# Optimization experiments

Measured on AMD Instinct MI355X. Metric: run time of the kernel, lower is better.

## Reference

```python
import jax, jax.numpy as jnp
import numpy as np

EMBED = 256; HEADS = 8; LEVELS = 4; POINTS = 4; DIM = EMBED // HEADS


def _bilinear_gather(vflat, H, W, px, py):
    """grid_sample(mode='bilinear', padding='zeros', align_corners=False).
    vflat: (bs, heads, H*W, d); px, py: (bs, heads, nq, P) pixel coords.
    Returns (bs, heads, nq, P, d).
    """
    x0 = jnp.floor(px); y0 = jnp.floor(py)
    x1 = x0 + 1.0;      y1 = y0 + 1.0
    wx1 = px - x0; wx0 = 1.0 - wx1
    wy1 = py - y0; wy0 = 1.0 - wy1

    def corner(ix, iy, w):
        valid = (ix >= 0) & (ix <= W - 1) & (iy >= 0) & (iy <= H - 1)
        idx = (jnp.clip(iy, 0, H - 1) * W + jnp.clip(ix, 0, W - 1)).astype(jnp.int32)
        b, h, nq, P = idx.shape
        g = jnp.take_along_axis(vflat, idx.reshape(b, h, nq * P)[..., None], axis=2)
        g = g.reshape(b, h, nq, P, -1)
        return g * (w * valid)[..., None]

    return (corner(x0, y0, wx0 * wy0) + corner(x1, y0, wx1 * wy0)
            + corner(x0, y1, wx0 * wy1) + corner(x1, y1, wx1 * wy1))


def _ms_deform_attn(value4, shapes, loc, attn):
    """value4 (bs,nv,heads,D); loc (bs,nq,heads,L,P,2) in [0,1];
    attn (bs,nq,heads,L,P). Returns (bs,nq,heads*D)."""
    bs, nq = loc.shape[0], loc.shape[1]
    grids = 2.0 * loc - 1.0
    attn_t = jnp.transpose(attn, (0, 2, 1, 3, 4))  # (bs,heads,nq,L,P)
    out = jnp.zeros((bs, HEADS, nq, DIM), value4.dtype)
    start = 0
    for lvl in range(LEVELS):
        H, W = int(shapes[lvl, 0]), int(shapes[lvl, 1])
        v = value4[:, start:start + H * W]                 # (bs,HW,heads,D)
        vflat = jnp.transpose(v, (0, 2, 1, 3))             # (bs,heads,HW,D)
        g = jnp.transpose(grids[:, :, :, lvl], (0, 2, 1, 3, 4))  # (bs,heads,nq,P,2)
        px = (g[..., 0] + 1.0) * (W * 0.5) - 0.5
        py = (g[..., 1] + 1.0) * (H * 0.5) - 0.5
        sampled = _bilinear_gather(vflat, H, W, px, py)    # (bs,heads,nq,P,D)
        out = out + jnp.einsum('bhqpd,bhqp->bhqd', sampled, attn_t[:, :, :, lvl])
        start += H * W
    return jnp.transpose(out, (0, 2, 1, 3)).reshape(bs, nq, HEADS * DIM)


def _forward(query, value, query_pos, reference_points, last_reference_offsets,
             shapes, Wv, bv, Wo, bo, Wa, ba, Wout, bout):
    identity = query
    q = query + query_pos
    bs, nq, _ = q.shape
    nv = value.shape[1]
    v = (value @ Wv + bv).reshape(bs, nv, HEADS, DIM)
    off = (q @ Wo + bo).reshape(bs, nq, HEADS, LEVELS, POINTS, 2)
    attn = jax.nn.softmax((q @ Wa + ba).reshape(bs, nq, HEADS, LEVELS * POINTS), axis=-1)
    attn = attn.reshape(bs, nq, HEADS, LEVELS, POINTS)
    wh = jnp.asarray(np.asarray(shapes)[:, ::-1].copy(), jnp.float32)  # (L,2) as (w,h)
    loc = (reference_points[:, :, None, :, None, :]
           + off / wh[None, None, None, :, None, :]
           + last_reference_offsets[:, :, :, None, None, :])  # flow-guided per-head shift
    out = _ms_deform_attn(v, shapes, loc, attn)
    return out @ Wout + bout + identity  # dropout is identity at eval


def setup_inputs() -> dict:
    key = jax.random.key(0)
    ks = jax.random.split(key, 10)
    bs, nq = 8, 1200
    shapes = np.array([[92, 160], [46, 80], [23, 40], [12, 20]], np.int64)
    nv = int((shapes[:, 0] * shapes[:, 1]).sum())
    f = jnp.float32
    return {
        "query": jax.random.normal(ks[0], (bs, nq, EMBED), f),
        "value": jax.random.normal(ks[1], (bs, nv, EMBED), f),
        "query_pos": jax.random.normal(ks[2], (bs, nq, EMBED), f),
        "reference_points": jax.random.uniform(ks[3], (bs, nq, LEVELS, 2), f),
        "last_reference_offsets": jax.random.normal(ks[4], (bs, nq, HEADS, 2), f) * 0.02,
        "spatial_shapes": shapes,
        "Wv": jax.random.normal(ks[5], (EMBED, EMBED), f) * 0.02,
        "bv": jnp.zeros((EMBED,), f),
        "Wo": jax.random.normal(ks[6], (EMBED, HEADS * LEVELS * POINTS * 2), f) * 0.02,
        "bo": jax.random.normal(ks[7], (HEADS * LEVELS * POINTS * 2,), f) * 0.02,
        "Wa": jax.random.normal(ks[8], (EMBED, HEADS * LEVELS * POINTS), f) * 0.02,
        "ba": jnp.zeros((HEADS * LEVELS * POINTS,), f),
        "Wout": jax.random.normal(ks[9], (EMBED, EMBED), f) * 0.02,
        "bout": jnp.zeros((EMBED,), f),
    }


def reference(query, value, query_pos, reference_points, last_reference_offsets,
              spatial_shapes, Wv, bv, Wo, bo, Wa, ba, Wout, bout):
    return _forward(query, value, query_pos, reference_points, last_reference_offsets,
                    spatial_shapes, Wv, bv, Wo, bo, Wa, ba, Wout, bout)
```

## Files before the change

kernel.cpp:

```cpp
#include <hip/hip_runtime.h>
#include <math.h>

#define BS 8
#define NQ 1200
#define NV 19560
#define EMB 256

typedef __bf16 bf16;
typedef bf16 bf16x8 __attribute__((ext_vector_type(8)));
typedef float f32x4 __attribute__((ext_vector_type(4)));
typedef float f32x16 __attribute__((ext_vector_type(16)));

static __device__ __forceinline__ bf16x8 cvt8(float4 a, float4 b) {
    bf16x8 r;
    r[0] = (bf16)a.x; r[1] = (bf16)a.y; r[2] = (bf16)a.z; r[3] = (bf16)a.w;
    r[4] = (bf16)b.x; r[5] = (bf16)b.y; r[6] = (bf16)b.z; r[7] = (bf16)b.w;
    return r;
}

static __device__ __forceinline__ void gl16(const void* g, void* l) {
    __builtin_amdgcn_global_load_lds(
        (const __attribute__((address_space(1))) void*)g,
        (__attribute__((address_space(3))) void*)l, 16, 0, 0);
}

__global__ __launch_bounds__(256) void prep_k(
    const float* __restrict__ Wv, const float* __restrict__ Wo,
    const float* __restrict__ Wa, const float* __restrict__ Wout,
    const float* __restrict__ query, const float* __restrict__ qpos,
    bf16* __restrict__ Wv_p, bf16* __restrict__ Wo_p,
    bf16* __restrict__ Wa_p, bf16* __restrict__ Wout_p, bf16* __restrict__ qsum)
{
    int bid = blockIdx.x, tid = threadIdx.x;
    if (bid < 896) {
        const float* src; bf16* dst; int N, t0;
        if (bid < 256)      { src = Wv;   dst = Wv_p;   N = 256; t0 = bid * 256; }
        else if (bid < 512) { src = Wo;   dst = Wo_p;   N = 256; t0 = (bid - 256) * 256; }
        else if (bid < 640) { src = Wa;   dst = Wa_p;   N = 128; t0 = (bid - 512) * 256; }
        else                { src = Wout; dst = Wout_p; N = 256; t0 = (bid - 640) * 256; }
        int t = t0 + tid;
        int n = t >> 8, k = t & 255;
        dst[t] = (bf16)src[k * N + n];
    } else {
        int t = (bid - 896) * 256 + tid;
        qsum[t] = (bf16)(query[t] + qpos[t]);
    }
}

__global__ __launch_bounds__(256, 1) void vgemm_k(
    const float* __restrict__ A, const bf16* __restrict__ Bp,
    const float* __restrict__ bias, bf16* __restrict__ outB, int Mtiles)
{
    __shared__ __align__(16) bf16 sB[256 * 256];
    __shared__ __align__(16) float sA[2][64 * 64];
    const int tid = threadIdx.x;
    const int lane = tid & 63;
    const int w = tid >> 6;
    const int l32 = lane & 31;
    const int hi = lane >> 5;
    const int wr = w >> 1, wc = w & 1;
    const int tstride = gridDim.x;

#pragma unroll
    for (int i = 0; i < 32; ++i) {
        int s = i * 256 + tid;
        int r = s >> 5, p = s & 31, c = p ^ (r & 7);
        gl16(Bp + (size_t)r * 256 + c * 8, sB + ((size_t)i * 256 + w * 64) * 8);
    }

    const int rl = lane >> 4;
    const int sl = lane & 15;
    auto stageA = [&](int t, int kc, int buf) {
        const float* base = A + (size_t)t * 64 * 256 + kc * 64;
#pragma unroll
        for (int i = 0; i < 4; ++i) {
            int r = w * 16 + i * 4 + rl;
            int c = sl ^ (r & 7);
            gl16(base + (size_t)r * 256 + c * 4, &sA[buf][(w * 16 + i * 4) * 64]);
        }
    };

    int t = blockIdx.x;
    stageA(t, 0, 0);

    float bb[4];
#pragma unroll
    for (int ct = 0; ct < 4; ++ct) bb[ct] = bias[wc * 128 + ct * 32 + l32];

    __syncthreads();

    int cur = 0;
    const int ar = wr * 32 + l32;
    while (true) {
        f32x16 acc[4];
#pragma unroll
        for (int ct = 0; ct < 4; ++ct)
#pragma unroll
            for (int rg = 0; rg < 16; ++rg) acc[ct][rg] = 0.f;

        const bool last = (t + tstride >= Mtiles);
#pragma unroll
        for (int kc = 0; kc < 4; ++kc) {
            if (kc < 3)     stageA(t, kc + 1, cur ^ 1);
            else if (!last) stageA(t + tstride, 0, cur ^ 1);
#pragma unroll
            for (int ks2 = 0; ks2 < 4; ++ks2) {
                int c0 = ks2 * 4 + hi * 2;
                float4 a0 = *(const float4*)&sA[cur][ar * 64 + ((c0    ) ^ (ar & 7)) * 4];
                float4 a1 = *(const float4*)&sA[cur][ar * 64 + ((c0 + 1) ^ (ar & 7)) * 4];
                bf16x8 af = cvt8(a0, a1);
                int p = ((kc * 4 + ks2) * 2 + hi) ^ (l32 & 7);
#pragma unroll
                for (int ct = 0; ct < 4; ++ct) {
                    int br = wc * 128 + ct * 32 + l32;
                    bf16x8 bfr = *(const bf16x8*)(sB + (size_t)br * 256 + p * 8);
                    acc[ct] = __builtin_amdgcn_mfma_f32_32x32x16_bf16(af, bfr, acc[ct], 0, 0, 0);
                }
            }
            __syncthreads();
            cur ^= 1;
        }

#pragma unroll
        for (int ct = 0; ct < 4; ++ct) {
            int col = wc * 128 + ct * 32 + l32;
#pragma unroll
            for (int rg = 0; rg < 16; ++rg) {
                int row = t * 64 + wr * 32 + (rg & 3) + 8 * (rg >> 2) + 4 * hi;
                outB[(size_t)row * 256 + col] = (bf16)(acc[ct][rg] + bb[ct]);
            }
        }
        if (last) break;
        t += tstride;
    }
}

template <int NS, int NB, bool HAS_RES, bool OUT_BF16>
__global__ __launch_bounds__(256, 2) void gemm3_k(
    const bf16* __restrict__ Ah, const bf16* __restrict__ Bp,
    const float* __restrict__ bias, const float* __restrict__ res,
    float* __restrict__ outF, bf16* __restrict__ outB, int Mtiles)
{
    constexpr int CT = NB / 16;
    __shared__ __align__(16) bf16 sB[NB * 256];
    const int tid = threadIdx.x;
    const int lane = tid & 63;
    const int w = tid >> 6;
    const int l16 = lane & 15;
    const int qd = lane >> 4;
    const int col0 = (blockIdx.x & 1) * NB;
    const int tstride = gridDim.x >> 1;
    const bf16* Bsrc = Bp + (size_t)col0 * 256;

    uint4 curH[8], nxtH[8];
    auto loadA = [&](int t, uint4* dH) {
        size_t rb = ((size_t)t * 64 + w * 16 + l16) * 256;
#pragma unroll
        for (int kc = 0; kc < 8; ++kc)
            dH[kc] = *(const uint4*)(Ah + rb + kc * 32 + qd * 8);
    };

    int tile = blockIdx.x >> 1;
    if (tile < Mtiles) loadA(tile, curH);

#pragma unroll
    for (int i = 0; i < NB * 32 / 256; ++i) {
        int s = i * 256 + tid;
        int r = s >> 5, p = s & 31, c = p ^ (r & 7);
        gl16(Bsrc + (size_t)r * 256 + c * 8, sB + (size_t)(i * 256 + w * 64) * 8);
    }
    __syncthreads();

    for (; tile < Mtiles; tile += tstride) {
        int nt = tile + tstride;
        if (nt < Mtiles) loadA(nt, nxtH);

        f32x4 acc[CT];
#pragma unroll
        for (int c = 0; c < CT; ++c) acc[c] = (f32x4){0.f, 0.f, 0.f, 0.f};
#pragma unroll
        for (int kc = 0; kc < 8; ++kc) {
            bf16x8 af = *(const bf16x8*)&curH[kc];
#pragma unroll
            for (int ct = 0; ct < CT; ++ct) {
                int brow = ct * 16 + l16;
                int chunk = (kc * 4 + qd) ^ (l16 & 7);
                bf16x8 bfr = *(const bf16x8*)(sB + (size_t)brow * 256 + chunk * 8);
                acc[ct] = __builtin_amdgcn_mfma_f32_16x16x32_bf16(af, bfr, acc[ct], 0, 0, 0);
            }
        }
#pragma unroll
        for (int ct = 0; ct < CT; ++ct) {
            int col = col0 + ct * 16 + l16;
            float bbv = bias[col];
#pragma unroll
            for (int r = 0; r < 4; ++r) {
                int row = tile * 64 + w * 16 + qd * 4 + r;
                size_t idx = (size_t)row * NS + col;
                float v = acc[ct][r] + bbv;
                if (HAS_RES) v += res[idx];
                if (OUT_BF16) outB[idx] = (bf16)v;
                else          outF[idx] = v;
            }
        }
#pragma unroll
        for (int i = 0; i < 8; ++i) curH[i] = nxtH[i];
    }
}

static __device__ __forceinline__ void b8f(uint4 u, float* f) {
    f[0] = __uint_as_float(u.x << 16); f[1] = __uint_as_float(u.x & 0xffff0000u);
    f[2] = __uint_as_float(u.y << 16); f[3] = __uint_as_float(u.y & 0xffff0000u);
    f[4] = __uint_as_float(u.z << 16); f[5] = __uint_as_float(u.z & 0xffff0000u);
    f[6] = __uint_as_float(u.w << 16); f[7] = __uint_as_float(u.w & 0xffff0000u);
}

__global__ __launch_bounds__(256) void sample4_k(
    const bf16* __restrict__ vv, const float* __restrict__ offb,
    const float* __restrict__ attnb, const float* __restrict__ refp,
    const float* __restrict__ lref, bf16* __restrict__ outb)
{
    const int cH[4] = {92, 46, 23, 12};
    const int cW[4] = {160, 80, 40, 20};
    const int cS[4] = {0, 14720, 18400, 19320};
    const int w = threadIdx.x >> 6;
    const int lane = threadIdx.x & 63;
    const int wid = blockIdx.x * 4 + w;
    const int bq = wid >> 3, h = wid & 7;
    const int b = bq / NQ;
    const int p = lane >> 2, dg = lane & 3;
    const int lvl = p >> 2;

    float logit = attnb[(size_t)bq * 128 + h * 16 + p];
    float mx = logit;
#pragma unroll
    for (int s = 4; s < 64; s <<= 1) mx = fmaxf(mx, __shfl_xor(mx, s));
    float e = __expf(logit - mx);
    float ssum = e;
#pragma unroll
    for (int s = 4; s < 64; s <<= 1) ssum += __shfl_xor(ssum, s);
    float wgt = e / ssum;

    const int Hh = cH[lvl], Ww = cW[lvl];
    float ox = offb[(size_t)bq * 256 + h * 32 + p * 2];
    float oy = offb[(size_t)bq * 256 + h * 32 + p * 2 + 1];
    float rx = refp[(size_t)bq * 8 + lvl * 2];
    float ry = refp[(size_t)bq * 8 + lvl * 2 + 1];
    float lrx = lref[(size_t)bq * 16 + h * 2];
    float lry = lref[(size_t)bq * 16 + h * 2 + 1];

    float px = (rx + ox / (float)Ww + lrx) * (float)Ww - 0.5f;
    float py = (ry + oy / (float)Hh + lry) * (float)Hh - 0.5f;
    float x0f = floorf(px), y0f = floorf(py);
    int x0 = (int)x0f, y0 = (int)y0f;
    float wx1 = px - x0f, wx0 = 1.f - wx1;
    float wy1 = py - y0f, wy0 = 1.f - wy1;
    bool xa = (unsigned)x0 < (unsigned)Ww, xb = (unsigned)(x0 + 1) < (unsigned)Ww;
    bool ya = (unsigned)y0 < (unsigned)Hh, yb = (unsigned)(y0 + 1) < (unsigned)Hh;
    int xc0 = min(max(x0, 0), Ww - 1), xc1 = min(max(x0 + 1, 0), Ww - 1);
    int yc0 = min(max(y0, 0), Hh - 1), yc1 = min(max(y0 + 1, 0), Hh - 1);
    float w00 = wgt * wx0 * wy0 * (float)(xa && ya);
    float w01 = wgt * wx1 * wy0 * (float)(xb && ya);
    float w10 = wgt * wx0 * wy1 * (float)(xa && yb);
    float w11 = wgt * wx1 * wy1 * (float)(xb && yb);

    const bf16* vb = vv + ((size_t)b * NV + cS[lvl]) * 256 + h * 32 + dg * 8;
    uint4 g00 = *(const uint4*)(vb + ((size_t)yc0 * Ww + xc0) * 256);
    uint4 g01 = *(const uint4*)(vb + ((size_t)yc0 * Ww + xc1) * 256);
    uint4 g10 = *(const uint4*)(vb + ((size_t)yc1 * Ww + xc0) * 256);
    uint4 g11 = *(const uint4*)(vb + ((size_t)yc1 * Ww + xc1) * 256);

    float acc[8], f[8];
    b8f(g00, f);
#pragma unroll
    for (int j = 0; j < 8; j++) acc[j] = w00 * f[j];
    b8f(g01, f);
#pragma unroll
    for (int j = 0; j < 8; j++) acc[j] = fmaf(w01, f[j], acc[j]);
    b8f(g10, f);
#pragma unroll
    for (int j = 0; j < 8; j++) acc[j] = fmaf(w10, f[j], acc[j]);
    b8f(g11, f);
#pragma unroll
    for (int j = 0; j < 8; j++) acc[j] = fmaf(w11, f[j], acc[j]);

#pragma unroll
    for (int s = 4; s < 64; s <<= 1)
#pragma unroll
        for (int j = 0; j < 8; j++) acc[j] += __shfl_xor(acc[j], s);

    if (p == 0) {
        bf16x8 o;
#pragma unroll
        for (int j = 0; j < 8; j++) o[j] = (bf16)acc[j];
        *(bf16x8*)(outb + (size_t)bq * 256 + h * 32 + dg * 8) = o;
    }
}

extern "C" void kernel_launch(void* const* d_in, const int* in_sizes, int n_in,
                              void* d_out, int out_size, void* d_ws, size_t ws_size,
                              hipStream_t stream) {
    (void)in_sizes; (void)n_in; (void)out_size; (void)ws_size;
    const float* query = (const float*)d_in[0];
    const float* value = (const float*)d_in[1];
    const float* qpos  = (const float*)d_in[2];
    const float* refp  = (const float*)d_in[3];
    const float* lref  = (const float*)d_in[4];
    const float* Wv   = (const float*)d_in[6];
    const float* bv   = (const float*)d_in[7];
    const float* Wo   = (const float*)d_in[8];
    const float* bo   = (const float*)d_in[9];
    const float* Wa   = (const float*)d_in[10];
    const float* ba   = (const float*)d_in[11];
    const float* Wout = (const float*)d_in[12];
    const float* bout = (const float*)d_in[13];

    char* ws = (char*)d_ws;
    bf16*  Wv_p   = (bf16*)(ws + 0);
    bf16*  Wo_p   = (bf16*)(ws + 131072);
    bf16*  Wa_p   = (bf16*)(ws + 262144);
    bf16*  Wout_p = (bf16*)(ws + 327680);
    bf16*  qsum   = (bf16*)(ws + 458752);
    float* off_b  = (float*)(ws + 5373952);
    float* attn_b = (float*)(ws + 15204352);
    bf16*  tsa_b  = (bf16*)(ws + 20119552);
    bf16*  v_b    = (bf16*)(ws + 25034752);

    prep_k<<<10496, 256, 0, stream>>>(Wv, Wo, Wa, Wout, query, qpos,
                                      Wv_p, Wo_p, Wa_p, Wout_p, qsum);

    vgemm_k<<<256, 256, 0, stream>>>(value, Wv_p, bv, v_b, (BS * NV) / 64);
    gemm3_k<256, 128, false, false><<<300, 256, 0, stream>>>(
        qsum, Wo_p, bo, nullptr, off_b, nullptr, (BS * NQ) / 64);
    gemm3_k<128, 64, false, false><<<300, 256, 0, stream>>>(
        qsum, Wa_p, ba, nullptr, attn_b, nullptr, (BS * NQ) / 64);
    sample4_k<<<(BS * NQ * 8) / 4, 256, 0, stream>>>(v_b, off_b, attn_b, refp, lref, tsa_b);
    gemm3_k<256, 128, true, false><<<300, 256, 0, stream>>>(
        tsa_b, Wout_p, bout, query, (float*)d_out, nullptr, (BS * NQ) / 64);
}
```

Baseline: 391.4 us.

## Stream weight tiles per K-chunk in value GEMM instead of persistent full-B LDS

The value projection GEMM no longer keeps the whole 256x256 bf16 weight matrix resident in LDS with a persistent grid of 256 blocks. Each block now handles one 64-row tile, and A and B are streamed together in 32-wide K chunks with double buffering. LDS per block drops from about 160 KB to about 48 KB, so up to 3 blocks can share a CU and hide latency. In exchange every block re-reads the weight matrix from L2, there are 2445 blocks instead of 256, and there are twice as many barriers per tile.

```diff
diff --git a/kernel.cpp b/kernel.cpp
--- a/kernel.cpp
+++ b/kernel.cpp
@@ -47,91 +47,96 @@
     }
 }
 
-__global__ __launch_bounds__(256, 1) void vgemm_k(
+__global__ __launch_bounds__(256, 3) void vgemm_k(
     const float* __restrict__ A, const bf16* __restrict__ Bp,
-    const float* __restrict__ bias, bf16* __restrict__ outB, int Mtiles)
+    const float* __restrict__ bias, bf16* __restrict__ outB)
 {
-    __shared__ __align__(16) bf16 sB[256 * 256];
-    __shared__ __align__(16) float sA[2][64 * 64];
+    __shared__ __align__(16) float sA[2][64 * 32];
+    __shared__ __align__(16) bf16  sB2[2][256 * 32];
     const int tid = threadIdx.x;
     const int lane = tid & 63;
     const int w = tid >> 6;
     const int l32 = lane & 31;
     const int hi = lane >> 5;
     const int wr = w >> 1, wc = w & 1;
-    const int tstride = gridDim.x;
-
-#pragma unroll
-    for (int i = 0; i < 32; ++i) {
-        int s = i * 256 + tid;
-        int r = s >> 5, p = s & 31, c = p ^ (r & 7);
-        gl16(Bp + (size_t)r * 256 + c * 8, sB + ((size_t)i * 256 + w * 64) * 8);
-    }
-
-    const int rl = lane >> 4;
-    const int sl = lane & 15;
-    auto stageA = [&](int t, int kc, int buf) {
-        const float* base = A + (size_t)t * 64 * 256 + kc * 64;
+    const int t = blockIdx.x;
+
+    const int alr = lane >> 3, ap = lane & 7;
+    auto stageA = [&](int kc2, int buf) {
+        const float* base = A + (size_t)t * 64 * 256 + kc2 * 32;
+#pragma unroll
+        for (int i = 0; i < 2; ++i) {
+            int r = w * 16 + i * 8 + alr;
+            int c = ap ^ (r & 7);
+            gl16(base + (size_t)r * 256 + c * 4, &sA[buf][(w * 16 + i * 8) * 32]);
+        }
+    };
+    const int brp = lane >> 2, bsp = lane & 3;
+    const int blr = ((brp & 3) << 2) | (brp >> 2);
+    auto stageB = [&](int kc2, int buf) {
+        const bf16* base = Bp + kc2 * 32;
 #pragma unroll
         for (int i = 0; i < 4; ++i) {
-            int r = w * 16 + i * 4 + rl;
-            int c = sl ^ (r & 7);
-            gl16(base + (size_t)r * 256 + c * 4, &sA[buf][(w * 16 + i * 4) * 64]);
+            int g = w * 4 + i;
+            int gr = g * 16 + blr;
+            int gq = bsp ^ (gr & 3);
+            gl16(base + (size_t)gr * 256 + gq * 8, sB2[buf] + (size_t)g * 16 * 32);
         }
     };
 
-    int t = blockIdx.x;
-    stageA(t, 0, 0);
+    stageA(0, 0);
+    stageB(0, 0);
 
     float bb[4];
 #pragma unroll
     for (int ct = 0; ct < 4; ++ct) bb[ct] = bias[wc * 128 + ct * 32 + l32];
 
+    int brg_[4], brx_[4];
+#pragma unroll
+    for (int ct = 0; ct < 4; ++ct) {
+        int br = wc * 128 + ct * 32 + l32;
+        brg_[ct] = (br & ~15) | (((br & 3) << 2) | ((br >> 2) & 3));
+        brx_[ct] = br & 3;
+    }
+
     __syncthreads();
 
+    f32x16 acc[4];
+#pragma unroll
+    for (int ct = 0; ct < 4; ++ct)
+#pragma unroll
+        for (int rg = 0; rg < 16; ++rg) acc[ct][rg] = 0.f;
+
+    const int ar = wr * 32 + l32;
     int cur = 0;
-    const int ar = wr * 32 + l32;
-    while (true) {
-        f32x16 acc[4];
-#pragma unroll
-        for (int ct = 0; ct < 4; ++ct)
-#pragma unroll
-            for (int rg = 0; rg < 16; ++rg) acc[ct][rg] = 0.f;
-
-        const bool last = (t + tstride >= Mtiles);
-#pragma unroll
-        for (int kc = 0; kc < 4; ++kc) {
-            if (kc < 3)     stageA(t, kc + 1, cur ^ 1);
-            else if (!last) stageA(t + tstride, 0, cur ^ 1);
-#pragma unroll
-            for (int ks2 = 0; ks2 < 4; ++ks2) {
-                int c0 = ks2 * 4 + hi * 2;
-                float4 a0 = *(const float4*)&sA[cur][ar * 64 + ((c0    ) ^ (ar & 7)) * 4];
-                float4 a1 = *(const float4*)&sA[cur][ar * 64 + ((c0 + 1) ^ (ar & 7)) * 4];
-                bf16x8 af = cvt8(a0, a1);
-                int p = ((kc * 4 + ks2) * 2 + hi) ^ (l32 & 7);
-#pragma unroll
-                for (int ct = 0; ct < 4; ++ct) {
-                    int br = wc * 128 + ct * 32 + l32;
-                    bf16x8 bfr = *(const bf16x8*)(sB + (size_t)br * 256 + p * 8);
-                    acc[ct] = __builtin_amdgcn_mfma_f32_32x32x16_bf16(af, bfr, acc[ct], 0, 0, 0);
-                }
+#pragma unroll
+    for (int kc2 = 0; kc2 < 8; ++kc2) {
+        if (kc2 < 7) { stageA(kc2 + 1, cur ^ 1); stageB(kc2 + 1, cur ^ 1); }
+#pragma unroll
+        for (int ks = 0; ks < 2; ++ks) {
+            int c0 = ks * 4 + hi * 2;
+            float4 a0 = *(const float4*)&sA[cur][ar * 32 + ((c0    ) ^ (ar & 7)) * 4];
+            float4 a1 = *(const float4*)&sA[cur][ar * 32 + ((c0 + 1) ^ (ar & 7)) * 4];
+            bf16x8 af = cvt8(a0, a1);
+            int q = ks * 2 + hi;
+#pragma unroll
+            for (int ct = 0; ct < 4; ++ct) {
+                bf16x8 bfr = *(const bf16x8*)(sB2[cur] + brg_[ct] * 32 + (q ^ brx_[ct]) * 8);
+                acc[ct] = __builtin_amdgcn_mfma_f32_32x32x16_bf16(af, bfr, acc[ct], 0, 0, 0);
             }
-            __syncthreads();
-            cur ^= 1;
-        }
-
-#pragma unroll
-        for (int ct = 0; ct < 4; ++ct) {
-            int col = wc * 128 + ct * 32 + l32;
-#pragma unroll
-            for (int rg = 0; rg < 16; ++rg) {
-                int row = t * 64 + wr * 32 + (rg & 3) + 8 * (rg >> 2) + 4 * hi;
-                outB[(size_t)row * 256 + col] = (bf16)(acc[ct][rg] + bb[ct]);
-            }
-        }
-        if (last) break;
-        t += tstride;
+        }
+        __syncthreads();
+        cur ^= 1;
+    }
+
+#pragma unroll
+    for (int ct = 0; ct < 4; ++ct) {
+        int col = wc * 128 + ct * 32 + l32;
+#pragma unroll
+        for (int rg = 0; rg < 16; ++rg) {
+            int row = t * 64 + wr * 32 + (rg & 3) + 8 * (rg >> 2) + 4 * hi;
+            outB[(size_t)row * 256 + col] = (bf16)(acc[ct][rg] + bb[ct]);
+        }
     }
 }
 
@@ -329,7 +334,7 @@
     prep_k<<<10496, 256, 0, stream>>>(Wv, Wo, Wa, Wout, query, qpos,
                                       Wv_p, Wo_p, Wa_p, Wout_p, qsum);
 
-    vgemm_k<<<256, 256, 0, stream>>>(value, Wv_p, bv, v_b, (BS * NV) / 64);
+    vgemm_k<<<(BS * NV) / 64, 256, 0, stream>>>(value, Wv_p, bv, v_b);
     gemm3_k<256, 128, false, false><<<300, 256, 0, stream>>>(
         qsum, Wo_p, bo, nullptr, off_b, nullptr, (BS * NQ) / 64);
     gemm3_k<128, 64, false, false><<<300, 256, 0, stream>>>(
```

Result: slower. 406.6 us (+3.9%).

## Give each wave private A staging and drop block barriers in value GEMM

Applied to the files above, without the earlier changes.

The value-projection GEMM now lets each wave own a 16-row strip of the A tile in its own LDS region and compute all 256 output columns with 16x16x32 MFMAs. The old layout was a 2x2 wave grid using 32x32 MFMAs. Because each wave only reads A rows it loaded itself, per-k-chunk __syncthreads are replaced with s_waitcnt vmcnt counters, and two k-chunks are prefetched at a time. This removes block-wide barrier stalls, but each wave must now read the whole B matrix from LDS for every A fragment and holds 16 accumulators. The vmcnt-based waits rely on the global_load_lds ordering per wave being correct.

```diff
diff --git a/kernel.cpp b/kernel.cpp
--- a/kernel.cpp
+++ b/kernel.cpp
@@ -51,15 +51,13 @@
     const float* __restrict__ A, const bf16* __restrict__ Bp,
     const float* __restrict__ bias, bf16* __restrict__ outB, int Mtiles)
 {
-    __shared__ __align__(16) bf16 sB[256 * 256];
-    __shared__ __align__(16) float sA[2][64 * 64];
+    __shared__ __align__(16) bf16  sB[256 * 256];
+    __shared__ __align__(16) float sA[4 * 2 * 1024];
     const int tid = threadIdx.x;
     const int lane = tid & 63;
     const int w = tid >> 6;
-    const int l32 = lane & 31;
-    const int hi = lane >> 5;
-    const int wr = w >> 1, wc = w & 1;
-    const int tstride = gridDim.x;
+    const int l16 = lane & 15;
+    const int qd = lane >> 4;
 
 #pragma unroll
     for (int i = 0; i < 32; ++i) {
@@ -68,71 +66,83 @@
         gl16(Bp + (size_t)r * 256 + c * 8, sB + ((size_t)i * 256 + w * 64) * 8);
     }
 
-    const int rl = lane >> 4;
-    const int sl = lane & 15;
+    float* sAw = sA + w * 2048;
+    const int lr4 = lane >> 4, sl = lane & 15;
+    int aoff[4];
+#pragma unroll
+    for (int i = 0; i < 4; ++i) {
+        int lr = i * 4 + lr4;
+        aoff[i] = (w * 16 + lr) * 256 + ((sl ^ (lr & 7)) * 4);
+    }
     auto stageA = [&](int t, int kc, int buf) {
-        const float* base = A + (size_t)t * 64 * 256 + kc * 64;
-#pragma unroll
-        for (int i = 0; i < 4; ++i) {
-            int r = w * 16 + i * 4 + rl;
-            int c = sl ^ (r & 7);
-            gl16(base + (size_t)r * 256 + c * 4, &sA[buf][(w * 16 + i * 4) * 64]);
+        const float* base = A + (size_t)t * 16384 + kc * 64;
+#pragma unroll
+        for (int i = 0; i < 4; ++i)
+            gl16(base + aoff[i], sAw + buf * 1024 + i * 256);
+    };
+
+    int t = blockIdx.x;
+    stageA(t, 0, 0);
+    stageA(t, 1, 1);
+
+    float bb[16];
+#pragma unroll
+    for (int ct = 0; ct < 16; ++ct) bb[ct] = bias[ct * 16 + l16];
+
+    __syncthreads();
+
+    const int akey = l16 & 7;
+    f32x4 acc[16];
+
+    auto compute = [&](int kc, int buf) {
+        const float* ar = sAw + buf * 1024 + l16 * 64;
+#pragma unroll
+        for (int ks = 0; ks < 2; ++ks) {
+            int kg = kc * 2 + ks;
+            int s  = ks * 8 + qd * 2;
+            float4 a0 = *(const float4*)(ar + ((s    ) ^ akey) * 4);
+            float4 a1 = *(const float4*)(ar + ((s + 1) ^ akey) * 4);
+            bf16x8 af = cvt8(a0, a1);
+#pragma unroll
+            for (int ct = 0; ct < 16; ++ct) {
+                int brow = ct * 16 + l16;
+                bf16x8 bfr = *(const bf16x8*)(sB + (size_t)brow * 256 +
+                                              ((kg * 4 + qd) ^ (brow & 7)) * 8);
+                acc[ct] = __builtin_amdgcn_mfma_f32_16x16x32_bf16(af, bfr, acc[ct], 0, 0, 0);
+            }
         }
     };
 
-    int t = blockIdx.x;
-    stageA(t, 0, 0);
-
-    float bb[4];
-#pragma unroll
-    for (int ct = 0; ct < 4; ++ct) bb[ct] = bias[wc * 128 + ct * 32 + l32];
-
-    __syncthreads();
-
-    int cur = 0;
-    const int ar = wr * 32 + l32;
+#define VM_WAIT4 asm volatile("s_waitcnt vmcnt(4)" ::: "memory")
+#define VM_WAIT0 asm volatile("s_waitcnt vmcnt(0)" ::: "memory")
+
     while (true) {
-        f32x16 acc[4];
-#pragma unroll
-        for (int ct = 0; ct < 4; ++ct)
-#pragma unroll
-            for (int rg = 0; rg < 16; ++rg) acc[ct][rg] = 0.f;
-
-        const bool last = (t + tstride >= Mtiles);
-#pragma unroll
-        for (int kc = 0; kc < 4; ++kc) {
-            if (kc < 3)     stageA(t, kc + 1, cur ^ 1);
-            else if (!last) stageA(t + tstride, 0, cur ^ 1);
-#pragma unroll
-            for (int ks2 = 0; ks2 < 4; ++ks2) {
-                int c0 = ks2 * 4 + hi * 2;
-                float4 a0 = *(const float4*)&sA[cur][ar * 64 + ((c0    ) ^ (ar & 7)) * 4];
-                float4 a1 = *(const float4*)&sA[cur][ar * 64 + ((c0 + 1) ^ (ar & 7)) * 4];
-                bf16x8 af = cvt8(a0, a1);
-                int p = ((kc * 4 + ks2) * 2 + hi) ^ (l32 & 7);
-#pragma unroll
-                for (int ct = 0; ct < 4; ++ct) {
-                    int br = wc * 128 + ct * 32 + l32;
-                    bf16x8 bfr = *(const bf16x8*)(sB + (size_t)br * 256 + p * 8);
-                    acc[ct] = __builtin_amdgcn_mfma_f32_32x32x16_bf16(af, bfr, acc[ct], 0, 0, 0);
-                }
-            }
-            __syncthreads();
-            cur ^= 1;
-        }
-
-#pragma unroll
-        for (int ct = 0; ct < 4; ++ct) {
-            int col = wc * 128 + ct * 32 + l32;
-#pragma unroll
-            for (int rg = 0; rg < 16; ++rg) {
-                int row = t * 64 + wr * 32 + (rg & 3) + 8 * (rg >> 2) + 4 * hi;
-                outB[(size_t)row * 256 + col] = (bf16)(acc[ct][rg] + bb[ct]);
+#pragma unroll
+        for (int ct = 0; ct < 16; ++ct) acc[ct] = (f32x4){0.f, 0.f, 0.f, 0.f};
+
+        VM_WAIT4; compute(0, 0); stageA(t, 2, 0);
+        VM_WAIT4; compute(1, 1); stageA(t, 3, 1);
+        VM_WAIT4; compute(2, 0);
+        VM_WAIT0; compute(3, 1);
+
+#pragma unroll
+        for (int ct = 0; ct < 16; ++ct) {
+            int col = ct * 16 + l16;
+#pragma unroll
+            for (int r = 0; r < 4; ++r) {
+                int row = t * 64 + w * 16 + qd * 4 + r;
+                outB[(size_t)row * 256 + col] = (bf16)(acc[ct][r] + bb[ct]);
             }
         }
-        if (last) break;
-        t += tstride;
-    }
+
+        int tn = t + gridDim.x;
+        if (tn >= Mtiles) break;
+        stageA(tn, 0, 0);
+        stageA(tn, 1, 1);
+        t = tn;
+    }
+#undef VM_WAIT4
+#undef VM_WAIT0
 }
 
 template <int NS, int NB, bool HAS_RES, bool OUT_BF16>
```

After: 392.4 us. About the same (+0.2%).
